# Optimization experiments

Measured on AMD Instinct MI355X. Metric: run time of the kernel, lower is better.

The kernel has to match this reference:

```python
import jax, jax.numpy as jnp
import numpy as np

N_HEAD = 8
HID = 256
V_DIM = HID // N_HEAD
NQ = 2048
NK = 2048
BATCH = 16
LOCALITY = 50.0  # percentile threshold; <=100 enables local masking


def setup_inputs() -> dict:
    key = jax.random.key(0)
    k1, k2, k3, k4 = jax.random.split(key, 4)
    m_dist = jax.random.uniform(k1, (N_HEAD, NQ, NK), dtype=jnp.float32)
    x = jax.random.normal(k2, (BATCH, NK, HID), dtype=jnp.float32)
    r = jax.random.normal(k3, (N_HEAD, 1, 1), dtype=jnp.float32)
    weight = jax.random.normal(k4, (N_HEAD, HID, V_DIM), dtype=jnp.float32) / jnp.sqrt(
        jnp.float32(HID)
    )
    return {"m_dist": m_dist, "x": x, "r": r, "weight": weight}


def reference(m_dist, x, r, weight):
    # distance scaling: tan(pi/4 * (1-eps) * (1 + sin(r))), per head
    scale = jnp.tan(0.25 * jnp.pi * (1.0 - 1e-07) * (1.0 + jnp.sin(r)))  # [H,1,1]
    scaled = m_dist * scale  # [H, Nq, Nk]
    # percentile-threshold local masking per (head, query) row
    thr = jnp.percentile(scaled, LOCALITY, axis=-1, keepdims=True)  # [H, Nq, 1]
    scaled = jnp.where(scaled <= thr, scaled, jnp.inf)
    att = jax.nn.softmax(-scaled, axis=-1)  # [H, Nq, Nk]
    value = jnp.einsum("bnj,hjk->bhnk", x, weight)  # [B, H, Nk, v]
    out = jnp.einsum("hjn,bhnk->bhjk", att, value)  # [B, H, Nq, v]
    out = jnp.transpose(out, (0, 2, 1, 3)).reshape(out.shape[0], out.shape[2], -1)
    return jax.nn.gelu(out)  # [B, Nq, HID]
```

## Files before the change

kernel.cpp:

```cpp
#include <hip/hip_runtime.h>
#include <hip/hip_bf16.h>

#define NH   8
#define HID  256
#define VD   32
#define NQ   2048
#define NKK  2048
#define NB   16
#define NN   512

typedef short bf16x8 __attribute__((ext_vector_type(8)));
typedef float f32x4 __attribute__((ext_vector_type(4)));

__device__ inline unsigned short f2bf(float f) {
  unsigned int u = __float_as_uint(f);
  u += 0x7FFFu + ((u >> 16) & 1u);
  return (unsigned short)(u >> 16);
}

__device__ inline void gload_lds16(const void* g, void* l) {
  __builtin_amdgcn_global_load_lds(
      (const __attribute__((address_space(1))) void*)g,
      (__attribute__((address_space(3))) void*)l, 16, 0, 0);
}

__device__ inline float gelu_f(float x) {
  float u2 = 1.5957691216057308f * (x + 0.044715f * x * x * x);
  float e = __expf(u2);
  return 0.5f * x * (1.0f + (e - 1.0f) / (e + 1.0f));
}


__global__ __launch_bounds__(256) void value_kernel(
    const float* __restrict__ w, const float* __restrict__ x,
    unsigned short* __restrict__ vT) {
  const int vb  = blockIdx.x;
  const int hvt = vb & 1;
  const int kt  = (vb >> 1) & 15;
  const int b   = vb >> 5;
  const int m0 = hvt * 128;
  const int n0 = kt * 128;
  const int t = threadIdx.x;
  const int lane = t & 63, wid = t >> 6;
  const int wr = wid >> 1, wc = wid & 1;

  __shared__ __align__(16) unsigned short As[128 * 32];
  __shared__ __align__(16) unsigned short Bs[128 * 32];

  const int arow = t >> 1;
  const int ahalf = t & 1;
  const int hh = (m0 + arow) >> 5, avv = (m0 + arow) & 31;
  const float* wbase = w + ((size_t)hh * HID + ahalf * 16) * VD + avv;
  const int ac = (arow >> 1) & 3;
  unsigned short* wA0 = (unsigned short*)((char*)As + arow * 64 + (((2 * ahalf) ^ ac) * 16));
  unsigned short* wA1 = (unsigned short*)((char*)As + arow * 64 + (((2 * ahalf + 1) ^ ac) * 16));

  const int brow = t >> 1, bj = (t & 1) * 16;
  const float* gB = x + ((size_t)b * NKK + n0 + brow) * HID + bj;
  const int bc = (brow >> 1) & 3;
  const int bs0 = (2 * (t & 1)) ^ bc;
  unsigned short* lB0 = Bs + brow * 32 + bs0 * 8;
  unsigned short* lB1 = Bs + brow * 32 + (bs0 ^ 1) * 8;

  f32x4 acc[4][4];
#pragma unroll
  for (int i = 0; i < 4; ++i)
#pragma unroll
    for (int j = 0; j < 4; ++j) acc[i][j] = (f32x4){0.f, 0.f, 0.f, 0.f};

  const int fr = lane & 15;
  const int kb = (((lane >> 4) ^ ((fr >> 1) & 3)) * 16);
  const char* baseA = (const char*)As + (wr * 64 + fr) * 64 + kb;
  const char* baseB = (const char*)Bs + (wc * 64 + fr) * 64 + kb;

  f32x4 p0 = *(const f32x4*)(gB + 0);
  f32x4 p1 = *(const f32x4*)(gB + 4);
  f32x4 p2 = *(const f32x4*)(gB + 8);
  f32x4 p3 = *(const f32x4*)(gB + 12);

  for (int kk = 0; kk < HID / 32; ++kk) {
    float av[16];
#pragma unroll
    for (int e = 0; e < 16; ++e) av[e] = wbase[((size_t)kk * 32 + e) * VD];

    f32x4 c0 = p0, c1 = p1, c2 = p2, c3 = p3;
    if (kk < HID / 32 - 1) {
      const float* nb = gB + (kk + 1) * 32;
      p0 = *(const f32x4*)(nb + 0);
      p1 = *(const f32x4*)(nb + 4);
      p2 = *(const f32x4*)(nb + 8);
      p3 = *(const f32x4*)(nb + 12);
    }
    uint4 qa0, qa1;
    qa0.x = (unsigned)f2bf(av[0]) | ((unsigned)f2bf(av[1]) << 16);
    qa0.y = (unsigned)f2bf(av[2]) | ((unsigned)f2bf(av[3]) << 16);
    qa0.z = (unsigned)f2bf(av[4]) | ((unsigned)f2bf(av[5]) << 16);
    qa0.w = (unsigned)f2bf(av[6]) | ((unsigned)f2bf(av[7]) << 16);
    qa1.x = (unsigned)f2bf(av[8]) | ((unsigned)f2bf(av[9]) << 16);
    qa1.y = (unsigned)f2bf(av[10]) | ((unsigned)f2bf(av[11]) << 16);
    qa1.z = (unsigned)f2bf(av[12]) | ((unsigned)f2bf(av[13]) << 16);
    qa1.w = (unsigned)f2bf(av[14]) | ((unsigned)f2bf(av[15]) << 16);
    *(uint4*)wA0 = qa0;
    *(uint4*)wA1 = qa1;

    uint4 pk0, pk1;
    pk0.x = (unsigned)f2bf(c0[0]) | ((unsigned)f2bf(c0[1]) << 16);
    pk0.y = (unsigned)f2bf(c0[2]) | ((unsigned)f2bf(c0[3]) << 16);
    pk0.z = (unsigned)f2bf(c1[0]) | ((unsigned)f2bf(c1[1]) << 16);
    pk0.w = (unsigned)f2bf(c1[2]) | ((unsigned)f2bf(c1[3]) << 16);
    pk1.x = (unsigned)f2bf(c2[0]) | ((unsigned)f2bf(c2[1]) << 16);
    pk1.y = (unsigned)f2bf(c2[2]) | ((unsigned)f2bf(c2[3]) << 16);
    pk1.z = (unsigned)f2bf(c3[0]) | ((unsigned)f2bf(c3[1]) << 16);
    pk1.w = (unsigned)f2bf(c3[2]) | ((unsigned)f2bf(c3[3]) << 16);
    *(uint4*)lB0 = pk0;
    *(uint4*)lB1 = pk1;

    __syncthreads();

    bf16x8 a[4], bfr[4];
#pragma unroll
    for (int i = 0; i < 4; ++i) a[i] = *(const bf16x8*)(baseA + i * 16 * 64);
#pragma unroll
    for (int j = 0; j < 4; ++j) bfr[j] = *(const bf16x8*)(baseB + j * 16 * 64);
#pragma unroll
    for (int i = 0; i < 4; ++i)
#pragma unroll
      for (int j = 0; j < 4; ++j)
        acc[i][j] = __builtin_amdgcn_mfma_f32_16x16x32_bf16(a[i], bfr[j], acc[i][j], 0, 0, 0);
    __syncthreads();
  }

  const int hvb = m0 + wr * 64 + (lane >> 4) * 4;
  const int kc0 = n0 + wc * 64 + (lane & 15);
#pragma unroll
  for (int i = 0; i < 4; ++i) {
#pragma unroll
    for (int j = 0; j < 4; ++j) {
      int kc = kc0 + j * 16;
#pragma unroll
      for (int e = 0; e < 4; ++e) {
        int hv = hvb + i * 16 + e;
        int h = hv >> 5, v = hv & 31;
        vT[((size_t)h * NN + b * VD + v) * NKK + kc] = f2bf(acc[i][j][e]);
      }
    }
  }
}

__global__ __launch_bounds__(256) void att_kernel(
    const float* __restrict__ m_dist, const float* __restrict__ r,
    unsigned short* __restrict__ att) {
  const int t = threadIdx.x;
  const int w = t >> 6;
  const int lane = t & 63;
  const int row = (blockIdx.x << 2) | w;
  const int h = row >> 11;

  __shared__ unsigned int histS[4][260];
  __shared__ float collS[4][192];
  __shared__ unsigned int minS[4];
  __shared__ float wsumS[4];
  __shared__ float vabS[4][2];

  unsigned int* hist = histS[w];
  float* coll = collS[w];

  const float C = (float)(0.25 * 3.141592653589793 * (1.0 - 1e-7));
  float sc = tanf(C * (1.0f + sinf(r[h])));

  *(uint4*)&hist[lane * 4] = (uint4){0u, 0u, 0u, 0u};
  if (lane == 0) { minS[w] = 0xFFFFFFFFu; wsumS[w] = 0.f; }

  const float* md = m_dist + (size_t)row * NKK + 4 * lane;
  f32x4 m4[8];
#pragma unroll
  for (int k = 0; k < 8; ++k) m4[k] = *(const f32x4*)(md + 256 * k);

  float t16[16];
#pragma unroll
  for (int i = 0; i < 16; ++i) t16[i] = fminf(m4[i >> 1][(i & 1) * 2], m4[i >> 1][(i & 1) * 2 + 1]);
#pragma unroll
  for (int s = 8; s; s >>= 1)
#pragma unroll
    for (int i = 0; i < s; ++i) t16[i] = fminf(t16[i], t16[i + s]);
  atomicMin(&minS[w], __float_as_uint(t16[0]));

#pragma unroll
  for (int k = 0; k < 8; ++k)
#pragma unroll
    for (int e = 0; e < 4; ++e) {
      int bin = min(max((int)(m4[k][e] * 256.0f), 0), 255);
      atomicAdd(&hist[bin], 1u);
    }

  asm volatile("s_waitcnt lgkmcnt(0)" ::: "memory");
  uint4 hc = *(const uint4*)&hist[lane * 4];
  unsigned c0 = hc.x, c1 = hc.x + hc.y, c2 = c1 + hc.z, c3 = c2 + hc.w;
  unsigned g = c3;
  unsigned incl = g;
#pragma unroll
  for (int off = 1; off < 64; off <<= 1) {
    unsigned y = __shfl_up(incl, off);
    if (lane >= off) incl += y;
  }
  unsigned excl = incl - g;

  unsigned long long ba1 = __ballot(incl >= 1024u);
  int glA = __ffsll((unsigned long long)ba1) - 1;
  unsigned eA = __shfl(excl, glA);
  unsigned a0 = __shfl(excl + c0, glA), a1 = __shfl(excl + c1, glA), a2 = __shfl(excl + c2, glA);
  int bA; unsigned below;
  if (a0 >= 1024u)      { bA = glA * 4 + 0; below = eA; }
  else if (a1 >= 1024u) { bA = glA * 4 + 1; below = a0; }
  else if (a2 >= 1024u) { bA = glA * 4 + 2; below = a1; }
  else                  { bA = glA * 4 + 3; below = a2; }
  unsigned long long ba2 = __ballot(incl >= 1025u);
  int glB = __ffsll((unsigned long long)ba2) - 1;
  unsigned e0 = __shfl(excl + c0, glB), e1 = __shfl(excl + c1, glB), e2 = __shfl(excl + c2, glB);
  int bB = (e0 >= 1025u) ? glB * 4 : (e1 >= 1025u) ? glB * 4 + 1
                                   : (e2 >= 1025u) ? glB * 4 + 2 : glB * 4 + 3;

  const unsigned long long below_me = (lane == 0) ? 0ull : (~0ull >> (64 - lane));
  unsigned base = 0;
#pragma unroll
  for (int k = 0; k < 8; ++k)
#pragma unroll
    for (int e = 0; e < 4; ++e) {
      float v = m4[k][e];
      int bin = min(max((int)(v * 256.0f), 0), 255);
      bool pred = (bin >= bA && bin <= bB);
      unsigned long long mask = __ballot(pred);
      if (pred) {
        unsigned idx = base + (unsigned)__popcll(mask & below_me);
        if (idx < 192u) coll[idx] = v;
      }
      base += (unsigned)__popcll(mask);
    }
  const int n = (int)min(base, 192u);
  asm volatile("s_waitcnt lgkmcnt(0)" ::: "memory");

  const int ra = 1023 - (int)below, rb = 1024 - (int)below;
  for (int idx = lane; idx < n; idx += 64) {
    float v = coll[idx];
    int rank = 0;
    for (int j2 = 0; j2 < n; ++j2) {
      float u = coll[j2];
      rank += (u < v || (u == v && j2 < idx)) ? 1 : 0;
    }
    if (rank == ra) vabS[w][0] = v;
    if (rank == rb) vabS[w][1] = v;
  }
  asm volatile("s_waitcnt lgkmcnt(0)" ::: "memory");

  float thr = 0.5f * (vabS[w][0] * sc) + 0.5f * (vabS[w][1] * sc);
  float minscaled = __uint_as_float(minS[w]) * sc;

  float ws = 0.f;
#pragma unroll
  for (int k = 0; k < 8; ++k)
#pragma unroll
    for (int e = 0; e < 4; ++e) {
      float s = m4[k][e] * sc;
      float x = (s <= thr) ? __expf(minscaled - s) : 0.f;
      m4[k][e] = x;
      ws += x;
    }
  atomicAdd(&wsumS[w], ws);
  asm volatile("s_waitcnt lgkmcnt(0)" ::: "memory");
  float inv = 1.0f / wsumS[w];

  unsigned short* ao = att + (size_t)row * NKK + 4 * lane;
#pragma unroll
  for (int k = 0; k < 8; ++k) {
    uint2 pk;
    pk.x = (unsigned)f2bf(m4[k][0] * inv) | ((unsigned)f2bf(m4[k][1] * inv) << 16);
    pk.y = (unsigned)f2bf(m4[k][2] * inv) | ((unsigned)f2bf(m4[k][3] * inv) << 16);
    *(uint2*)(ao + 256 * k) = pk;
  }
}

__global__ __launch_bounds__(256) void gemm_kernel(
    const unsigned short* __restrict__ att, const unsigned short* __restrict__ vT,
    float* __restrict__ out) {
  const int bid = blockIdx.x;
  const int h = bid & 7;
  const int tile = bid >> 3;
  const int qt = tile >> 2, nt = tile & 3;
  const int q0 = qt * 128, n0 = nt * 128;
  const int t = threadIdx.x;
  const int lane = t & 63, wid = t >> 6;
  const int wr = wid >> 1, wc = wid & 1;

  __shared__ __align__(16) unsigned short As[4][128 * 32];
  __shared__ __align__(16) unsigned short Bs[4][128 * 32];

  const int rowL = t >> 2;
  const int cb = (((t & 3) ^ ((t >> 3) & 3)) * 8);

  const unsigned short* gA = att + ((size_t)h * NQ + q0 + rowL) * NKK + cb;
  const unsigned short* gB = vT + ((size_t)h * NN + n0 + rowL) * NKK + cb;
  const int ldsOff = t * 16;

#define STAGE(BI, KT) do {                                                  \
    const unsigned short* a_ = gA + (KT) * 32;                              \
    const unsigned short* b_ = gB + (KT) * 32;                              \
    char* lA_ = (char*)As[(BI)] + ldsOff;                                   \
    char* lB_ = (char*)Bs[(BI)] + ldsOff;                                   \
    gload_lds16(a_, lA_);                                                   \
    gload_lds16(a_ + (size_t)64 * NKK, lA_ + 4096);                         \
    gload_lds16(b_, lB_);                                                   \
    gload_lds16(b_ + (size_t)64 * NKK, lB_ + 4096);                         \
  } while (0)

  f32x4 acc[4][4];
#pragma unroll
  for (int i = 0; i < 4; ++i)
#pragma unroll
    for (int j = 0; j < 4; ++j) acc[i][j] = (f32x4){0.f, 0.f, 0.f, 0.f};

  const int fr = lane & 15;
  const int kb = (((lane >> 4) ^ ((fr >> 1) & 3)) * 16);
  const int fragOff = (wr * 64 + fr) * 64 + kb;
  const int fragOffB = (wc * 64 + fr) * 64 + kb;

  STAGE(0, 0);
  STAGE(1, 1);
  STAGE(2, 2);
  asm volatile("s_waitcnt vmcnt(8)\n\ts_barrier" ::: "memory");

  for (int kt = 0; kt < 64; kt += 4) {
#pragma unroll
    for (int u = 0; u < 4; ++u) {
      const char* bA = (const char*)As[u] + fragOff;
      const char* bB = (const char*)Bs[u] + fragOffB;
      bf16x8 a[4], b[4];
#pragma unroll
      for (int i = 0; i < 4; ++i) a[i] = *(const bf16x8*)(bA + i * 1024);
#pragma unroll
      for (int j = 0; j < 4; ++j) b[j] = *(const bf16x8*)(bB + j * 1024);
      STAGE((u + 3) & 3, (kt + u + 3) & 63);
      __builtin_amdgcn_s_setprio(1);
#pragma unroll
      for (int i = 0; i < 4; ++i)
#pragma unroll
        for (int j = 0; j < 4; ++j)
          acc[i][j] = __builtin_amdgcn_mfma_f32_16x16x32_bf16(a[i], b[j], acc[i][j], 0, 0, 0);
      __builtin_amdgcn_s_setprio(0);
      asm volatile("s_waitcnt vmcnt(8)\n\ts_barrier" ::: "memory");
    }
  }
  asm volatile("s_waitcnt vmcnt(0)" ::: "memory");
#undef STAGE

  const int orow = q0 + wr * 64 + (lane >> 4) * 4;
  const int ocol0 = n0 + wc * 64 + (lane & 15);
#pragma unroll
  for (int i = 0; i < 4; ++i) {
#pragma unroll
    for (int j = 0; j < 4; ++j) {
      int ncol = ocol0 + j * 16;
      int bb = ncol >> 5, vv = ncol & 31;
      float* op = out + ((size_t)bb * NQ + orow + i * 16) * HID + h * VD + vv;
#pragma unroll
      for (int e = 0; e < 4; ++e) op[(size_t)e * HID] = gelu_f(acc[i][j][e]);
    }
  }
}

extern "C" void kernel_launch(void* const* d_in, const int* in_sizes, int n_in,
                              void* d_out, int out_size, void* d_ws, size_t ws_size,
                              hipStream_t stream) {
  const float* m_dist = (const float*)d_in[0];
  const float* x      = (const float*)d_in[1];
  const float* r      = (const float*)d_in[2];
  const float* weight = (const float*)d_in[3];
  float* out = (float*)d_out;

  unsigned short* att = (unsigned short*)d_ws;
  unsigned short* vT  = (unsigned short*)((char*)d_ws + (size_t)NH * NQ * NKK * 2);

  value_kernel<<<dim3(512), dim3(256), 0, stream>>>(weight, x, vT);
  att_kernel<<<dim3(NH * NQ / 4), dim3(256), 0, stream>>>(m_dist, r, att);
  gemm_kernel<<<dim3(NH * 64), dim3(256), 0, stream>>>(att, vT, out);
}
```

Measured before the change: 106.1 us.

## Fuse softmax exponentiation into GEMM A-tile load with deferred row normalization

The attention kernel now only computes a per-row threshold and minimum, stored as float2 stats. The GEMM reads fp32 m_dist directly and computes the masked exponentials on the fly into LDS as bf16. It accumulates row sums and applies 1/sum in the GELU epilogue. This removes the materialized bf16 attention matrix (its write and re-read). In exchange, each GEMM block rereads fp32 m_dist at twice the bytes per element, redoes the exp work once per n-tile, and drops the 4-stage async LDS pipeline for a single-buffered loop synchronized with __syncthreads.

After: 125.4 us, median of 2. 18.3% more time.

```diff
diff --git a/kernel.cpp b/kernel.cpp
--- a/kernel.cpp
+++ b/kernel.cpp
@@ -147,9 +147,9 @@
   }
 }
 
-__global__ __launch_bounds__(256) void att_kernel(
+__global__ __launch_bounds__(256) void stats_kernel(
     const float* __restrict__ m_dist, const float* __restrict__ r,
-    unsigned short* __restrict__ att) {
+    float2* __restrict__ stats) {
   const int t = threadIdx.x;
   const int w = t >> 6;
   const int lane = t & 63;
@@ -159,7 +159,6 @@
   __shared__ unsigned int histS[4][260];
   __shared__ float collS[4][192];
   __shared__ unsigned int minS[4];
-  __shared__ float wsumS[4];
   __shared__ float vabS[4][2];
 
   unsigned int* hist = histS[w];
@@ -169,7 +168,7 @@
   float sc = tanf(C * (1.0f + sinf(r[h])));
 
   *(uint4*)&hist[lane * 4] = (uint4){0u, 0u, 0u, 0u};
-  if (lane == 0) { minS[w] = 0xFFFFFFFFu; wsumS[w] = 0.f; }
+  if (lane == 0) minS[w] = 0xFFFFFFFFu;
 
   const float* md = m_dist + (size_t)row * NKK + 4 * lane;
   f32x4 m4[8];
@@ -252,35 +251,16 @@
   }
   asm volatile("s_waitcnt lgkmcnt(0)" ::: "memory");
 
-  float thr = 0.5f * (vabS[w][0] * sc) + 0.5f * (vabS[w][1] * sc);
-  float minscaled = __uint_as_float(minS[w]) * sc;
-
-  float ws = 0.f;
-#pragma unroll
-  for (int k = 0; k < 8; ++k)
-#pragma unroll
-    for (int e = 0; e < 4; ++e) {
-      float s = m4[k][e] * sc;
-      float x = (s <= thr) ? __expf(minscaled - s) : 0.f;
-      m4[k][e] = x;
-      ws += x;
-    }
-  atomicAdd(&wsumS[w], ws);
-  asm volatile("s_waitcnt lgkmcnt(0)" ::: "memory");
-  float inv = 1.0f / wsumS[w];
-
-  unsigned short* ao = att + (size_t)row * NKK + 4 * lane;
-#pragma unroll
-  for (int k = 0; k < 8; ++k) {
-    uint2 pk;
-    pk.x = (unsigned)f2bf(m4[k][0] * inv) | ((unsigned)f2bf(m4[k][1] * inv) << 16);
-    pk.y = (unsigned)f2bf(m4[k][2] * inv) | ((unsigned)f2bf(m4[k][3] * inv) << 16);
-    *(uint2*)(ao + 256 * k) = pk;
+  if (lane == 0) {
+    float thr = 0.5f * (vabS[w][0] * sc) + 0.5f * (vabS[w][1] * sc);
+    float ms = __uint_as_float(minS[w]) * sc;
+    stats[row] = make_float2(thr, ms);
   }
 }
 
 __global__ __launch_bounds__(256) void gemm_kernel(
-    const unsigned short* __restrict__ att, const unsigned short* __restrict__ vT,
+    const float* __restrict__ m_dist, const float* __restrict__ r,
+    const float2* __restrict__ stats, const unsigned short* __restrict__ vT,
     float* __restrict__ out) {
   const int bid = blockIdx.x;
   const int h = bid & 7;
@@ -291,26 +271,29 @@
   const int lane = t & 63, wid = t >> 6;
   const int wr = wid >> 1, wc = wid & 1;
 
-  __shared__ __align__(16) unsigned short As[4][128 * 32];
-  __shared__ __align__(16) unsigned short Bs[4][128 * 32];
+  __shared__ __align__(16) unsigned short As[128 * 32];
+  __shared__ __align__(16) unsigned short Bs[128 * 32];
+  __shared__ float wsumL[256];
+
+  const float C = (float)(0.25 * 3.141592653589793 * (1.0 - 1e-7));
+  const float sc = tanf(C * (1.0f + sinf(r[h])));
+
+  const int arow = t >> 1;
+  const int ahalf = t & 1;
+  const int grow = h * NQ + q0 + arow;
+  const float* gA = m_dist + (size_t)grow * NKK + ahalf * 16;
+  const float2 st = stats[grow];
+  const float thr = st.x, ms = st.y;
+  const int ac = (arow >> 1) & 3;
+  unsigned short* wA0 = (unsigned short*)((char*)As + arow * 64 + (((2 * ahalf) ^ ac) * 16));
+  unsigned short* wA1 = (unsigned short*)((char*)As + arow * 64 + (((2 * ahalf + 1) ^ ac) * 16));
 
   const int rowL = t >> 2;
   const int cb = (((t & 3) ^ ((t >> 3) & 3)) * 8);
-
-  const unsigned short* gA = att + ((size_t)h * NQ + q0 + rowL) * NKK + cb;
-  const unsigned short* gB = vT + ((size_t)h * NN + n0 + rowL) * NKK + cb;
-  const int ldsOff = t * 16;
-
-#define STAGE(BI, KT) do {                                                  \
-    const unsigned short* a_ = gA + (KT) * 32;                              \
-    const unsigned short* b_ = gB + (KT) * 32;                              \
-    char* lA_ = (char*)As[(BI)] + ldsOff;                                   \
-    char* lB_ = (char*)Bs[(BI)] + ldsOff;                                   \
-    gload_lds16(a_, lA_);                                                   \
-    gload_lds16(a_ + (size_t)64 * NKK, lA_ + 4096);                         \
-    gload_lds16(b_, lB_);                                                   \
-    gload_lds16(b_ + (size_t)64 * NKK, lB_ + 4096);                         \
-  } while (0)
+  const unsigned short* gB0 = vT + ((size_t)h * NN + n0 + rowL) * NKK + cb;
+  const unsigned short* gB1 = gB0 + (size_t)64 * NKK;
+  char* lB0 = (char*)Bs + t * 16;
+  char* lB1 = (char*)Bs + 4096 + t * 16;
 
   f32x4 acc[4][4];
 #pragma unroll
@@ -320,39 +303,72 @@
 
   const int fr = lane & 15;
   const int kb = (((lane >> 4) ^ ((fr >> 1) & 3)) * 16);
-  const int fragOff = (wr * 64 + fr) * 64 + kb;
-  const int fragOffB = (wc * 64 + fr) * 64 + kb;
-
-  STAGE(0, 0);
-  STAGE(1, 1);
-  STAGE(2, 2);
-  asm volatile("s_waitcnt vmcnt(8)\n\ts_barrier" ::: "memory");
-
-  for (int kt = 0; kt < 64; kt += 4) {
-#pragma unroll
-    for (int u = 0; u < 4; ++u) {
-      const char* bA = (const char*)As[u] + fragOff;
-      const char* bB = (const char*)Bs[u] + fragOffB;
-      bf16x8 a[4], b[4];
-#pragma unroll
-      for (int i = 0; i < 4; ++i) a[i] = *(const bf16x8*)(bA + i * 1024);
-#pragma unroll
-      for (int j = 0; j < 4; ++j) b[j] = *(const bf16x8*)(bB + j * 1024);
-      STAGE((u + 3) & 3, (kt + u + 3) & 63);
-      __builtin_amdgcn_s_setprio(1);
-#pragma unroll
-      for (int i = 0; i < 4; ++i)
-#pragma unroll
-        for (int j = 0; j < 4; ++j)
-          acc[i][j] = __builtin_amdgcn_mfma_f32_16x16x32_bf16(a[i], b[j], acc[i][j], 0, 0, 0);
-      __builtin_amdgcn_s_setprio(0);
-      asm volatile("s_waitcnt vmcnt(8)\n\ts_barrier" ::: "memory");
-    }
-  }
-  asm volatile("s_waitcnt vmcnt(0)" ::: "memory");
-#undef STAGE
-
-  const int orow = q0 + wr * 64 + (lane >> 4) * 4;
+  const char* baseA = (const char*)As + (wr * 64 + fr) * 64 + kb;
+  const char* baseB = (const char*)Bs + (wc * 64 + fr) * 64 + kb;
+
+  float psum = 0.f;
+
+  f32x4 p0 = *(const f32x4*)(gA + 0);
+  f32x4 p1 = *(const f32x4*)(gA + 4);
+  f32x4 p2 = *(const f32x4*)(gA + 8);
+  f32x4 p3 = *(const f32x4*)(gA + 12);
+
+  for (int kt = 0; kt < NKK / 32; ++kt) {
+    gload_lds16(gB0, lB0);
+    gload_lds16(gB1, lB1);
+    gB0 += 32; gB1 += 32;
+
+    f32x4 c0 = p0, c1 = p1, c2 = p2, c3 = p3;
+    if (kt < NKK / 32 - 1) {
+      const float* nb = gA + (kt + 1) * 32;
+      p0 = *(const f32x4*)(nb + 0);
+      p1 = *(const f32x4*)(nb + 4);
+      p2 = *(const f32x4*)(nb + 8);
+      p3 = *(const f32x4*)(nb + 12);
+    }
+    float pv[16];
+#pragma unroll
+    for (int e = 0; e < 4; ++e) {
+      float s0 = c0[e] * sc; pv[e]      = (s0 <= thr) ? __expf(ms - s0) : 0.f;
+      float s1 = c1[e] * sc; pv[4 + e]  = (s1 <= thr) ? __expf(ms - s1) : 0.f;
+      float s2 = c2[e] * sc; pv[8 + e]  = (s2 <= thr) ? __expf(ms - s2) : 0.f;
+      float s3 = c3[e] * sc; pv[12 + e] = (s3 <= thr) ? __expf(ms - s3) : 0.f;
+    }
+#pragma unroll
+    for (int e = 0; e < 16; ++e) psum += pv[e];
+
+    uint4 qa0, qa1;
+    qa0.x = (unsigned)f2bf(pv[0]) | ((unsigned)f2bf(pv[1]) << 16);
+    qa0.y = (unsigned)f2bf(pv[2]) | ((unsigned)f2bf(pv[3]) << 16);
+    qa0.z = (unsigned)f2bf(pv[4]) | ((unsigned)f2bf(pv[5]) << 16);
+    qa0.w = (unsigned)f2bf(pv[6]) | ((unsigned)f2bf(pv[7]) << 16);
+    qa1.x = (unsigned)f2bf(pv[8]) | ((unsigned)f2bf(pv[9]) << 16);
+    qa1.y = (unsigned)f2bf(pv[10]) | ((unsigned)f2bf(pv[11]) << 16);
+    qa1.z = (unsigned)f2bf(pv[12]) | ((unsigned)f2bf(pv[13]) << 16);
+    qa1.w = (unsigned)f2bf(pv[14]) | ((unsigned)f2bf(pv[15]) << 16);
+    *(uint4*)wA0 = qa0;
+    *(uint4*)wA1 = qa1;
+
+    __syncthreads();
+
+    bf16x8 a[4], bfr[4];
+#pragma unroll
+    for (int i = 0; i < 4; ++i) a[i] = *(const bf16x8*)(baseA + i * 16 * 64);
+#pragma unroll
+    for (int j = 0; j < 4; ++j) bfr[j] = *(const bf16x8*)(baseB + j * 16 * 64);
+#pragma unroll
+    for (int i = 0; i < 4; ++i)
+#pragma unroll
+      for (int j = 0; j < 4; ++j)
+        acc[i][j] = __builtin_amdgcn_mfma_f32_16x16x32_bf16(a[i], bfr[j], acc[i][j], 0, 0, 0);
+    __syncthreads();
+  }
+
+  wsumL[arow * 2 + ahalf] = psum;
+  __syncthreads();
+
+  const int lrow0 = wr * 64 + (lane >> 4) * 4;
+  const int orow = q0 + lrow0;
   const int ocol0 = n0 + wc * 64 + (lane & 15);
 #pragma unroll
   for (int i = 0; i < 4; ++i) {
@@ -362,7 +378,11 @@
       int bb = ncol >> 5, vv = ncol & 31;
       float* op = out + ((size_t)bb * NQ + orow + i * 16) * HID + h * VD + vv;
 #pragma unroll
-      for (int e = 0; e < 4; ++e) op[(size_t)e * HID] = gelu_f(acc[i][j][e]);
+      for (int e = 0; e < 4; ++e) {
+        int lr = lrow0 + i * 16 + e;
+        float inv = 1.0f / (wsumL[lr * 2] + wsumL[lr * 2 + 1]);
+        op[(size_t)e * HID] = gelu_f(acc[i][j][e] * inv);
+      }
     }
   }
 }
@@ -376,10 +396,10 @@
   const float* weight = (const float*)d_in[3];
   float* out = (float*)d_out;
 
-  unsigned short* att = (unsigned short*)d_ws;
-  unsigned short* vT  = (unsigned short*)((char*)d_ws + (size_t)NH * NQ * NKK * 2);
+  unsigned short* vT = (unsigned short*)d_ws;
+  float2* stats = (float2*)((char*)d_ws + (size_t)NH * NN * NKK * 2);
 
   value_kernel<<<dim3(512), dim3(256), 0, stream>>>(weight, x, vT);
-  att_kernel<<<dim3(NH * NQ / 4), dim3(256), 0, stream>>>(m_dist, r, att);
-  gemm_kernel<<<dim3(NH * 64), dim3(256), 0, stream>>>(att, vT, out);
-}
+  stats_kernel<<<dim3(NH * NQ / 4), dim3(256), 0, stream>>>(m_dist, r, stats);
+  gemm_kernel<<<dim3(NH * 64), dim3(256), 0, stream>>>(m_dist, r, stats, vT, out);
+}
```

## Split attention kernel into stats and P passes, defer softmax normalization to GEMM

Applied to the files above, without the earlier changes.

The fused attention kernel becomes two kernels. A stats kernel computes each row's percentile threshold and minimum. A second kernel re-reads m_dist, writes unnormalized exp weights in bf16, and writes per-row sums; normalization moves into the GEMM epilogue. This likely aims to shorten the heavy stats kernel and its register pressure, at the cost of reading m_dist twice (about 128MB more traffic) plus an extra launch.

Result: slower. 129.1 us (+21.8%).

```diff
diff --git a/kernel.cpp b/kernel.cpp
--- a/kernel.cpp
+++ b/kernel.cpp
@@ -147,9 +147,9 @@
   }
 }
 
-__global__ __launch_bounds__(256) void att_kernel(
+__global__ __launch_bounds__(256) void stats_kernel(
     const float* __restrict__ m_dist, const float* __restrict__ r,
-    unsigned short* __restrict__ att) {
+    float2* __restrict__ stats) {
   const int t = threadIdx.x;
   const int w = t >> 6;
   const int lane = t & 63;
@@ -159,7 +159,6 @@
   __shared__ unsigned int histS[4][260];
   __shared__ float collS[4][192];
   __shared__ unsigned int minS[4];
-  __shared__ float wsumS[4];
   __shared__ float vabS[4][2];
 
   unsigned int* hist = histS[w];
@@ -169,7 +168,7 @@
   float sc = tanf(C * (1.0f + sinf(r[h])));
 
   *(uint4*)&hist[lane * 4] = (uint4){0u, 0u, 0u, 0u};
-  if (lane == 0) { minS[w] = 0xFFFFFFFFu; wsumS[w] = 0.f; }
+  if (lane == 0) minS[w] = 0xFFFFFFFFu;
 
   const float* md = m_dist + (size_t)row * NKK + 4 * lane;
   f32x4 m4[8];
@@ -252,8 +251,31 @@
   }
   asm volatile("s_waitcnt lgkmcnt(0)" ::: "memory");
 
-  float thr = 0.5f * (vabS[w][0] * sc) + 0.5f * (vabS[w][1] * sc);
-  float minscaled = __uint_as_float(minS[w]) * sc;
+  if (lane == 0) {
+    float thr = 0.5f * (vabS[w][0] * sc) + 0.5f * (vabS[w][1] * sc);
+    float ms = __uint_as_float(minS[w]) * sc;
+    stats[row] = make_float2(thr, ms);
+  }
+}
+
+__global__ __launch_bounds__(256) void p_kernel(
+    const float* __restrict__ m_dist, const float* __restrict__ r,
+    const float2* __restrict__ stats, unsigned short* __restrict__ P,
+    float* __restrict__ wsum) {
+  const int w = threadIdx.x >> 6;
+  const int lane = threadIdx.x & 63;
+  const int row = (blockIdx.x << 2) | w;
+  const int h = row >> 11;
+
+  const float C = (float)(0.25 * 3.141592653589793 * (1.0 - 1e-7));
+  const float sc = tanf(C * (1.0f + sinf(r[h])));
+  const float2 st = stats[row];
+  const float thr = st.x, ms = st.y;
+
+  const float* md = m_dist + (size_t)row * NKK + 4 * lane;
+  f32x4 m4[8];
+#pragma unroll
+  for (int k = 0; k < 8; ++k) m4[k] = *(const f32x4*)(md + 256 * k);
 
   float ws = 0.f;
 #pragma unroll
@@ -261,27 +283,27 @@
 #pragma unroll
     for (int e = 0; e < 4; ++e) {
       float s = m4[k][e] * sc;
-      float x = (s <= thr) ? __expf(minscaled - s) : 0.f;
+      float x = (s <= thr) ? __expf(ms - s) : 0.f;
       m4[k][e] = x;
       ws += x;
     }
-  atomicAdd(&wsumS[w], ws);
-  asm volatile("s_waitcnt lgkmcnt(0)" ::: "memory");
-  float inv = 1.0f / wsumS[w];
-
-  unsigned short* ao = att + (size_t)row * NKK + 4 * lane;
+#pragma unroll
+  for (int off = 32; off; off >>= 1) ws += __shfl_xor(ws, off);
+  if (lane == 0) wsum[row] = ws;
+
+  unsigned short* po = P + (size_t)row * NKK + 4 * lane;
 #pragma unroll
   for (int k = 0; k < 8; ++k) {
     uint2 pk;
-    pk.x = (unsigned)f2bf(m4[k][0] * inv) | ((unsigned)f2bf(m4[k][1] * inv) << 16);
-    pk.y = (unsigned)f2bf(m4[k][2] * inv) | ((unsigned)f2bf(m4[k][3] * inv) << 16);
-    *(uint2*)(ao + 256 * k) = pk;
+    pk.x = (unsigned)f2bf(m4[k][0]) | ((unsigned)f2bf(m4[k][1]) << 16);
+    pk.y = (unsigned)f2bf(m4[k][2]) | ((unsigned)f2bf(m4[k][3]) << 16);
+    *(uint2*)(po + 256 * k) = pk;
   }
 }
 
 __global__ __launch_bounds__(256) void gemm_kernel(
-    const unsigned short* __restrict__ att, const unsigned short* __restrict__ vT,
-    float* __restrict__ out) {
+    const unsigned short* __restrict__ P, const unsigned short* __restrict__ vT,
+    const float* __restrict__ wsum, float* __restrict__ out) {
   const int bid = blockIdx.x;
   const int h = bid & 7;
   const int tile = bid >> 3;
@@ -297,7 +319,7 @@
   const int rowL = t >> 2;
   const int cb = (((t & 3) ^ ((t >> 3) & 3)) * 8);
 
-  const unsigned short* gA = att + ((size_t)h * NQ + q0 + rowL) * NKK + cb;
+  const unsigned short* gA = P + ((size_t)h * NQ + q0 + rowL) * NKK + cb;
   const unsigned short* gB = vT + ((size_t)h * NN + n0 + rowL) * NKK + cb;
   const int ldsOff = t * 16;
 
@@ -354,6 +376,12 @@
 
   const int orow = q0 + wr * 64 + (lane >> 4) * 4;
   const int ocol0 = n0 + wc * 64 + (lane & 15);
+  float invr[4][4];
+#pragma unroll
+  for (int i = 0; i < 4; ++i)
+#pragma unroll
+    for (int e = 0; e < 4; ++e)
+      invr[i][e] = 1.0f / wsum[(size_t)h * NQ + orow + i * 16 + e];
 #pragma unroll
   for (int i = 0; i < 4; ++i) {
 #pragma unroll
@@ -362,7 +390,8 @@
       int bb = ncol >> 5, vv = ncol & 31;
       float* op = out + ((size_t)bb * NQ + orow + i * 16) * HID + h * VD + vv;
 #pragma unroll
-      for (int e = 0; e < 4; ++e) op[(size_t)e * HID] = gelu_f(acc[i][j][e]);
+      for (int e = 0; e < 4; ++e)
+        op[(size_t)e * HID] = gelu_f(acc[i][j][e] * invr[i][e]);
     }
   }
 }
@@ -376,10 +405,13 @@
   const float* weight = (const float*)d_in[3];
   float* out = (float*)d_out;
 
-  unsigned short* att = (unsigned short*)d_ws;
-  unsigned short* vT  = (unsigned short*)((char*)d_ws + (size_t)NH * NQ * NKK * 2);
-
+  unsigned short* P  = (unsigned short*)d_ws;
+  unsigned short* vT = (unsigned short*)((char*)d_ws + (size_t)NH * NQ * NKK * 2);
+  float2* stats = (float2*)((char*)d_ws + (size_t)NH * NQ * NKK * 2 + (size_t)NH * NN * NKK * 2);
+  float* wsum = (float*)((char*)stats + (size_t)NH * NQ * sizeof(float2));
+
+  stats_kernel<<<dim3(NH * NQ / 4), dim3(256), 0, stream>>>(m_dist, r, stats);
   value_kernel<<<dim3(512), dim3(256), 0, stream>>>(weight, x, vT);
-  att_kernel<<<dim3(NH * NQ / 4), dim3(256), 0, stream>>>(m_dist, r, att);
-  gemm_kernel<<<dim3(NH * 64), dim3(256), 0, stream>>>(att, vT, out);
-}
+  p_kernel<<<dim3(NH * NQ / 4), dim3(256), 0, stream>>>(m_dist, r, stats, P, wsum);
+  gemm_kernel<<<dim3(NH * 64), dim3(256), 0, stream>>>(P, vT, wsum, out);
+}
```
